# Kernel tuning notes

Hardware: AMD Instinct MI355X
Metric: run time of the kernel (lower is better)

## Reference

```python
import jax, jax.numpy as jnp
import numpy as np

B, N, D, H = 4, 2048, 256, 8
DH = D // H  # 32
EPS = 1e-5


def layernorm(x, g, b):
    mu = jnp.mean(x, axis=-1, keepdims=True)
    var = jnp.mean(jnp.square(x - mu), axis=-1, keepdims=True)
    return (x - mu) * jax.lax.rsqrt(var + EPS) * g + b


def setup_inputs() -> dict:
    key = jax.random.key(0)
    ks = jax.random.split(key, 16)
    s = 1.0 / np.sqrt(D)
    p = lambda k: jax.random.uniform(k, (D, D), jnp.float32, -s, s)
    return {
        "qdt": jax.random.normal(ks[0], (B, N, D), jnp.float32),
        "boxes": jax.random.normal(ks[1], (B, N, D), jnp.float32),
        "mask": jax.random.randint(ks[2], (N, N), 0, 2, jnp.int32),
        "Wq": p(ks[3]), "bq": jnp.zeros((D,), jnp.float32),
        "Wk": p(ks[4]), "bk": jnp.zeros((D,), jnp.float32),
        "Wv": p(ks[5]), "bv": jnp.zeros((D,), jnp.float32),
        "Wo": p(ks[6]), "bo": jnp.zeros((D,), jnp.float32),
        "W1": p(ks[7]), "b1": jnp.zeros((D,), jnp.float32),
        "W2": p(ks[8]), "b2": jnp.zeros((D,), jnp.float32),
        "g1": jnp.ones((D,), jnp.float32), "be1": jnp.zeros((D,), jnp.float32),
        "g2": jnp.ones((D,), jnp.float32), "be2": jnp.zeros((D,), jnp.float32),
    }


def reference(qdt, boxes, mask, Wq, bq, Wk, bk, Wv, bv, Wo, bo,
              W1, b1, W2, b2, g1, be1, g2, be2):
    # q = k = tgt = boxes + qdt  (dropout in eval mode -> identity)
    x = boxes + qdt  # [B,N,D]
    q = (x @ Wq + bq).reshape(B, N, H, DH)
    k = (x @ Wk + bk).reshape(B, N, H, DH)
    v = (x @ Wv + bv).reshape(B, N, H, DH)
    scores = jnp.einsum('bqhd,bkhd->bhqk', q, k) / np.sqrt(DH)
    # masked_fill(mask==0, -inf) then sigmoid  ==  sigmoid gated to 0 where masked
    attn = jnp.where(mask.astype(bool)[None, None, :, :],
                     jax.nn.sigmoid(scores), 0.0)
    o = jnp.einsum('bhqk,bkhd->bqhd', attn, v).reshape(B, N, D)
    attn_out = o @ Wo + bo
    tgt = layernorm(x + attn_out, g1, be1)
    ff = jax.nn.relu(tgt @ W1 + b1) @ W2 + b2
    tgt = layernorm(tgt + ff, g2, be2)
    return tgt
```

## Files before the change

### kernel.cpp

```cpp
#include <hip/hip_runtime.h>
#include <hip/hip_bf16.h>

typedef unsigned short u16;
typedef unsigned int u32;
typedef __attribute__((ext_vector_type(8))) short bf16x8;
typedef __attribute__((ext_vector_type(4))) float f32x4;

#define BB 4
#define NN 2048
#define DD 256
#define HH 8
#define LAMBDA 0.17677669529f

__device__ inline u16 bfu(float f) {
  __hip_bfloat16 h = __float2bfloat16(f);
  return *reinterpret_cast<u16*>(&h);
}
__device__ inline bf16x8 asfrag(uint4 v) { return __builtin_bit_cast(bf16x8, v); }

__global__ __launch_bounds__(256) void prep_kernel(
    const float* __restrict__ qdt, const float* __restrict__ boxes,
    const int* __restrict__ mask,
    const float* __restrict__ Wq, const float* __restrict__ Wk, const float* __restrict__ Wv,
    const float* __restrict__ Wo, const float* __restrict__ W1, const float* __restrict__ W2,
    const float* __restrict__ bq, const float* __restrict__ bk, const float* __restrict__ bv,
    float* __restrict__ xp, u16* __restrict__ xb, unsigned char* __restrict__ m8,
    u16* __restrict__ wqkvT, u16* __restrict__ woT, u16* __restrict__ w1T, u16* __restrict__ w2T,
    float* __restrict__ bqkv) {
  const int bid = blockIdx.x, t = threadIdx.x;
  if (bid < 2048) {
    int i = bid * 256 + t;
    int row = i >> 6, q = i & 63;
    float4 a = ((const float4*)qdt)[i];
    float4 b = ((const float4*)boxes)[i];
    float4 v = make_float4(a.x + b.x, a.y + b.y, a.z + b.z, a.w + b.w);
    ((ushort4*)xb)[i] = make_ushort4(bfu(v.x), bfu(v.y), bfu(v.z), bfu(v.w));
    float* xr = xp + (size_t)row * 256;
    xr[((4*q+0) & 15) * 16 + ((4*q+0) >> 4)] = v.x;
    xr[((4*q+1) & 15) * 16 + ((4*q+1) >> 4)] = v.y;
    xr[((4*q+2) & 15) * 16 + ((4*q+2) >> 4)] = v.z;
    xr[((4*q+3) & 15) * 16 + ((4*q+3) >> 4)] = v.w;
  } else if (bid < 6144) {
    int i = (bid - 2048) * 256 + t;
    int4 m = ((const int4*)mask)[i];
    ((uchar4*)m8)[i] = make_uchar4((unsigned char)m.x, (unsigned char)m.y,
                                   (unsigned char)m.z, (unsigned char)m.w);
  } else {
    int i = (bid - 6144) * 256 + t;
    if (i < 196608) {
      int n = i >> 8, k = i & 255;
      const float* src = (n < 256) ? Wq : (n < 512 ? Wk : Wv);
      wqkvT[i] = bfu(src[k * 256 + (n & 255)]);
    } else if (i < 262144) {
      int j = i - 196608; int n = j >> 8, k = j & 255;
      woT[j] = bfu(Wo[k * 256 + n]);
    } else if (i < 327680) {
      int j = i - 262144; int n = j >> 8, k = j & 255;
      w1T[j] = bfu(W1[k * 256 + n]);
    } else if (i < 393216) {
      int j = i - 327680; int n = j >> 8, k = j & 255;
      w2T[j] = bfu(W2[k * 256 + n]);
    } else if (i < 393984) {
      int n = i - 393216;
      bqkv[n] = (n < 256) ? bq[n] : (n < 512 ? bk[n - 256] : bv[n - 512]);
    }
  }
}

#define GEMM_BODY()                                                              \
  __shared__ u16 At[64][264];                                                    \
  __shared__ u16 Bs[64][264];                                                    \
  const int m0 = blockIdx.x * 64;                                                \
  const int n0 = blockIdx.y * 64;                                                \
  const int t = threadIdx.x;                                                     \
  {                                                                              \
    const int row = t >> 2, cb = (t & 3) * 64;                                   \
    const u16* ga = A  + (size_t)(m0 + row) * 256 + cb;                          \
    const u16* gb = Bt + (size_t)(n0 + row) * 256 + cb;                          \
    _Pragma("unroll")                                                            \
    for (int i = 0; i < 8; ++i) {                                                \
      *(int4*)&At[row][cb + i * 8] = *(const int4*)(ga + i * 8);                 \
      *(int4*)&Bs[row][cb + i * 8] = *(const int4*)(gb + i * 8);                 \
    }                                                                            \
  }                                                                              \
  __syncthreads();                                                               \
  const int w = t >> 6, l = t & 63, g = l >> 4, c = l & 15;                      \
  f32x4 acc[4] = {};                                                             \
  _Pragma("unroll")                                                              \
  for (int kk = 0; kk < 256; kk += 32) {                                         \
    bf16x8 af = *(const bf16x8*)&At[w * 16 + c][kk + g * 8];                     \
    _Pragma("unroll")                                                            \
    for (int j = 0; j < 4; ++j) {                                                \
      bf16x8 bfr = *(const bf16x8*)&Bs[j * 16 + c][kk + g * 8];                  \
      acc[j] = __builtin_amdgcn_mfma_f32_16x16x32_bf16(af, bfr, acc[j], 0, 0, 0);\
    }                                                                            \
  }

__global__ __launch_bounds__(256) void gemm_qk_kernel(
    const u16* __restrict__ A, const u16* __restrict__ Bt, const float* __restrict__ bias,
    u16* __restrict__ qout, u16* __restrict__ kout) {
  GEMM_BODY()
  if (n0 < 256) {
#pragma unroll
    for (int j = 0; j < 4; ++j)
#pragma unroll
      for (int r = 0; r < 4; ++r) {
        int m = m0 + w * 16 + g * 4 + r, n = n0 + j * 16 + c;
        qout[(size_t)m * 256 + n] = bfu((acc[j][r] + bias[n]) * LAMBDA);
      }
  } else {
#pragma unroll
    for (int j = 0; j < 4; ++j)
#pragma unroll
      for (int r = 0; r < 4; ++r) {
        int m = m0 + w * 16 + g * 4 + r, n = n0 + j * 16 + c;
        int ch = n - 256;
        kout[(size_t)((m >> 11) * 8 + (ch >> 5)) * 65536 + (size_t)(m & 2047) * 32 + (ch & 31)]
            = bfu(acc[j][r] + bias[n]);
      }
  }
}

__global__ __launch_bounds__(256) void gemm_vt_kernel(
    const u16* __restrict__ A, const u16* __restrict__ Bt, const float* __restrict__ bias,
    u16* __restrict__ vtout) {
  GEMM_BODY()
#pragma unroll
  for (int j = 0; j < 4; ++j)
#pragma unroll
    for (int r = 0; r < 4; ++r) {
      int m = m0 + w * 16 + g * 4 + r;
      int n = n0 + j * 16 + c;
      vtout[(size_t)m * 8192 + n] = bfu(acc[j][r] + bias[m]);
    }
}

__global__ __launch_bounds__(256) void attn_kernel(
    const u16* __restrict__ qb,
    const u16* __restrict__ kb,
    const u16* __restrict__ vtb,
    const unsigned char* __restrict__ m8,
    u16* __restrict__ ob) {
  __shared__ u32 Klds[2][64][20];
  __shared__ u32 Vlds[2][32][36];
  __shared__ unsigned char Mlds[2][64][64];
  __shared__ u32 Plds[4][16][36];

  const int bid = blockIdx.x;
  const int qt = bid & 31, h = (bid >> 5) & 7, b = bid >> 8;
  const int q0 = qt * 64;
  const int t = threadIdx.x, w = t >> 6, l = t & 63, g = l >> 4, c = l & 15;

  const bf16x8 qf = asfrag(*(const uint4*)(qb + (size_t)(b * NN + q0 + 16 * w + c) * 256 + h * 32 + 8 * g));
  f32x4 oacc[2] = {};

  const int srowK = t >> 2, ssegK = t & 3;
  const int srowV = t >> 3, ssegV = t & 7;
  const u16* kg = kb + (size_t)(b * 8 + h) * 65536 + srowK * 32 + ssegK * 8;
  const u16* vg = vtb + (size_t)(h * 32 + srowV) * 8192 + (size_t)b * NN + ssegV * 8;
  const unsigned char* mg = m8 + (size_t)(q0 + srowK) * NN + ssegK * 16;

  const int mb0 = (16 * ssegK + 8 * (srowK & 7)) & 63;
  const int mb1 = (mb0 + 8) & 63;

  uint4 krg = *(const uint4*)kg;
  uint4 vrg = *(const uint4*)vg;
  uint4 mrg = *(const uint4*)mg;
  *(uint4*)&Klds[0][srowK][ssegK * 4] = krg;
  *(uint4*)&Vlds[0][srowV][ssegV * 4] = vrg;
  *(uint2*)&Mlds[0][srowK][mb0] = make_uint2(mrg.x, mrg.y);
  *(uint2*)&Mlds[0][srowK][mb1] = make_uint2(mrg.z, mrg.w);
  __syncthreads();

  const f32x4 zf = {0.f, 0.f, 0.f, 0.f};
  u32* Pw = &Plds[w][0][0];

  for (int it = 0; it < 32; ++it) {
    const int cur = it & 1;
    if (it < 31) {
      const int kt = (it + 1) * 64;
      krg = *(const uint4*)(kg + (size_t)kt * 32);
      vrg = *(const uint4*)(vg + kt);
      mrg = *(const uint4*)(mg + kt);
    }
#pragma unroll
    for (int tt = 0; tt < 4; ++tt) {
      bf16x8 kf = asfrag(*(const uint4*)&Klds[cur][16 * tt + c][4 * g]);
      f32x4 s = __builtin_amdgcn_mfma_f32_16x16x32_bf16(kf, qf, zf, 0, 0, 0);
      u32 mdw = *(const u32*)&Mlds[cur][16 * w + c][(16 * tt + 4 * g + 8 * (c & 7)) & 63];
      float mf0 = (float)(mdw & 0xffu);
      float mf1 = (float)((mdw >> 8) & 0xffu);
      float mf2 = (float)((mdw >> 16) & 0xffu);
      float mf3 = (float)(mdw >> 24);
      float p0 = mf0 * __builtin_amdgcn_rcpf(1.f + __expf(-s[0]));
      float p1 = mf1 * __builtin_amdgcn_rcpf(1.f + __expf(-s[1]));
      float p2 = mf2 * __builtin_amdgcn_rcpf(1.f + __expf(-s[2]));
      float p3 = mf3 * __builtin_amdgcn_rcpf(1.f + __expf(-s[3]));
      u32 w0, w1;
      asm("v_cvt_pk_bf16_f32 %0, %1, %2" : "=v"(w0) : "v"(p0), "v"(p1));
      asm("v_cvt_pk_bf16_f32 %0, %1, %2" : "=v"(w1) : "v"(p2), "v"(p3));
      *(uint2*)&Pw[c * 36 + 8 * tt + 2 * g] = make_uint2(w0, w1);
    }
    asm volatile("s_waitcnt lgkmcnt(0)" ::: "memory");
    __builtin_amdgcn_sched_barrier(0);
#pragma unroll
    for (int kk = 0; kk < 2; ++kk) {
      bf16x8 pf = asfrag(*(const uint4*)&Pw[c * 36 + 16 * kk + 4 * g]);
#pragma unroll
      for (int d0 = 0; d0 < 2; ++d0) {
        bf16x8 vf = asfrag(*(const uint4*)&Vlds[cur][16 * d0 + c][16 * kk + 4 * g]);
        oacc[d0] = __builtin_amdgcn_mfma_f32_16x16x32_bf16(pf, vf, oacc[d0], 0, 0, 0);
      }
    }
    if (it < 31) {
      *(uint4*)&Klds[cur ^ 1][srowK][ssegK * 4] = krg;
      *(uint4*)&Vlds[cur ^ 1][srowV][ssegV * 4] = vrg;
      *(uint2*)&Mlds[cur ^ 1][srowK][mb0] = make_uint2(mrg.x, mrg.y);
      *(uint2*)&Mlds[cur ^ 1][srowK][mb1] = make_uint2(mrg.z, mrg.w);
    }
    __syncthreads();
  }

  const size_t obase = (size_t)(b * NN + q0 + 16 * w) * 256 + h * 32;
#pragma unroll
  for (int d0 = 0; d0 < 2; ++d0)
#pragma unroll
    for (int r = 0; r < 4; ++r)
      ob[obase + (size_t)(4 * g + r) * 256 + 16 * d0 + c] = bfu(oacc[d0][r]);
}

__global__ __launch_bounds__(64) void tail_kernel(
    const u16* __restrict__ obuf, const u16* __restrict__ woT,
    const u16* __restrict__ w1T, const u16* __restrict__ w2T,
    const float* __restrict__ xp,
    const float* __restrict__ bo, const float* __restrict__ b1, const float* __restrict__ b2,
    const float* __restrict__ g1, const float* __restrict__ be1,
    const float* __restrict__ g2, const float* __restrict__ be2,
    float* __restrict__ out) {
  __shared__ u16 A[16][264];
  __shared__ float T1[16][260];
  const int t = threadIdx.x, g = t >> 4, c = t & 15;
  const int m0 = blockIdx.x * 16;
  const f32x4 zf4 = {0.f, 0.f, 0.f, 0.f};

  {
    const int srow = t >> 2, sseg = t & 3;
#pragma unroll
    for (int i = 0; i < 8; ++i) {
      uint4 v = *(const uint4*)(obuf + (size_t)(m0 + srow) * 256 + (sseg + 4 * i) * 8);
      *(uint4*)&A[srow][(sseg + 4 * i) * 8] = v;
    }
  }
  asm volatile("s_waitcnt lgkmcnt(0)" ::: "memory");
  __builtin_amdgcn_sched_barrier(0);

  f32x4 acc[16];
  float s1[4], s2[4], mean[4], inv[4];

#pragma unroll
  for (int j = 0; j < 16; ++j) acc[j] = zf4;
#pragma unroll
  for (int kk = 0; kk < 256; kk += 32) {
    bf16x8 af = *(const bf16x8*)&A[c][kk + 8 * g];
#pragma unroll
    for (int j = 0; j < 16; ++j) {
      bf16x8 bfr = asfrag(*(const uint4*)(woT + (size_t)(16 * j + c) * 256 + kk + 8 * g));
      acc[j] = __builtin_amdgcn_mfma_f32_16x16x32_bf16(af, bfr, acc[j], 0, 0, 0);
    }
  }
  {
    float bov[16];
#pragma unroll
    for (int j = 0; j < 16; ++j) bov[j] = bo[16 * j + c];
#pragma unroll
    for (int r = 0; r < 4; ++r) {
      const float* xrow = xp + (size_t)(m0 + 4 * g + r) * 256 + c * 16;
      float4 xq0 = ((const float4*)xrow)[0], xq1 = ((const float4*)xrow)[1];
      float4 xq2 = ((const float4*)xrow)[2], xq3 = ((const float4*)xrow)[3];
      float xa[16] = {xq0.x, xq0.y, xq0.z, xq0.w, xq1.x, xq1.y, xq1.z, xq1.w,
                      xq2.x, xq2.y, xq2.z, xq2.w, xq3.x, xq3.y, xq3.z, xq3.w};
      float a1 = 0.f, a2 = 0.f;
#pragma unroll
      for (int j = 0; j < 16; ++j) {
        float z = acc[j][r] + bov[j] + xa[j];
        T1[4 * g + r][16 * j + c] = z;
        a1 += z; a2 += z * z;
      }
      s1[r] = a1; s2[r] = a2;
    }
  }
#pragma unroll
  for (int r = 0; r < 4; ++r) {
#pragma unroll
    for (int off = 1; off < 16; off <<= 1) {
      s1[r] += __shfl_xor(s1[r], off);
      s2[r] += __shfl_xor(s2[r], off);
    }
    mean[r] = s1[r] * (1.f / 256.f);
    inv[r] = rsqrtf(s2[r] * (1.f / 256.f) - mean[r] * mean[r] + 1e-5f);
  }
  asm volatile("s_waitcnt lgkmcnt(0)" ::: "memory");
  __builtin_amdgcn_sched_barrier(0);
#pragma unroll
  for (int j = 0; j < 16; ++j) {
    const int n = 16 * j + c;
    const float gv = g1[n], bev = be1[n];
#pragma unroll
    for (int r = 0; r < 4; ++r) {
      float v = (T1[4 * g + r][n] - mean[r]) * inv[r] * gv + bev;
      T1[4 * g + r][n] = v;
      A[4 * g + r][n] = bfu(v);
    }
  }
  asm volatile("s_waitcnt lgkmcnt(0)" ::: "memory");
  __builtin_amdgcn_sched_barrier(0);

#pragma unroll
  for (int j = 0; j < 16; ++j) acc[j] = zf4;
#pragma unroll
  for (int kk = 0; kk < 256; kk += 32) {
    bf16x8 af = *(const bf16x8*)&A[c][kk + 8 * g];
#pragma unroll
    for (int j = 0; j < 16; ++j) {
      bf16x8 bfr = asfrag(*(const uint4*)(w1T + (size_t)(16 * j + c) * 256 + kk + 8 * g));
      acc[j] = __builtin_amdgcn_mfma_f32_16x16x32_bf16(af, bfr, acc[j], 0, 0, 0);
    }
  }
  asm volatile("" ::: "memory");
  __builtin_amdgcn_sched_barrier(0);
#pragma unroll
  for (int j = 0; j < 16; ++j) {
    const int n = 16 * j + c;
    const float bv = b1[n];
#pragma unroll
    for (int r = 0; r < 4; ++r) {
      float v = acc[j][r] + bv;
      A[4 * g + r][n] = bfu(v > 0.f ? v : 0.f);
    }
  }
  asm volatile("s_waitcnt lgkmcnt(0)" ::: "memory");
  __builtin_amdgcn_sched_barrier(0);

#pragma unroll
  for (int j = 0; j < 16; ++j) acc[j] = zf4;
#pragma unroll
  for (int kk = 0; kk < 256; kk += 32) {
    bf16x8 af = *(const bf16x8*)&A[c][kk + 8 * g];
#pragma unroll
    for (int j = 0; j < 16; ++j) {
      bf16x8 bfr = asfrag(*(const uint4*)(w2T + (size_t)(16 * j + c) * 256 + kk + 8 * g));
      acc[j] = __builtin_amdgcn_mfma_f32_16x16x32_bf16(af, bfr, acc[j], 0, 0, 0);
    }
  }
  {
    float b2v[16];
#pragma unroll
    for (int j = 0; j < 16; ++j) b2v[j] = b2[16 * j + c];
#pragma unroll
    for (int r = 0; r < 4; ++r) {
      float a1 = 0.f, a2 = 0.f;
#pragma unroll
      for (int j = 0; j < 16; ++j) {
        float z = acc[j][r] + b2v[j] + T1[4 * g + r][16 * j + c];
        T1[4 * g + r][16 * j + c] = z;
        a1 += z; a2 += z * z;
      }
      s1[r] = a1; s2[r] = a2;
    }
  }
#pragma unroll
  for (int r = 0; r < 4; ++r) {
#pragma unroll
    for (int off = 1; off < 16; off <<= 1) {
      s1[r] += __shfl_xor(s1[r], off);
      s2[r] += __shfl_xor(s2[r], off);
    }
    mean[r] = s1[r] * (1.f / 256.f);
    inv[r] = rsqrtf(s2[r] * (1.f / 256.f) - mean[r] * mean[r] + 1e-5f);
  }
  asm volatile("s_waitcnt lgkmcnt(0)" ::: "memory");
  __builtin_amdgcn_sched_barrier(0);
#pragma unroll
  for (int j = 0; j < 16; ++j) {
    const int n = 16 * j + c;
    const float gv = g2[n], bev = be2[n];
#pragma unroll
    for (int r = 0; r < 4; ++r)
      out[(size_t)(m0 + 4 * g + r) * 256 + n] = (T1[4 * g + r][n] - mean[r]) * inv[r] * gv + bev;
  }
}

extern "C" void kernel_launch(void* const* d_in, const int* in_sizes, int n_in,
                              void* d_out, int out_size, void* d_ws, size_t ws_size,
                              hipStream_t stream) {
  const float* qdt   = (const float*)d_in[0];
  const float* boxes = (const float*)d_in[1];
  const int*   mask  = (const int*)d_in[2];
  const float* Wq = (const float*)d_in[3];
  const float* bq = (const float*)d_in[4];
  const float* Wk = (const float*)d_in[5];
  const float* bk = (const float*)d_in[6];
  const float* Wv = (const float*)d_in[7];
  const float* bv = (const float*)d_in[8];
  const float* Wo = (const float*)d_in[9];
  const float* bo = (const float*)d_in[10];
  const float* W1 = (const float*)d_in[11];
  const float* b1 = (const float*)d_in[12];
  const float* W2 = (const float*)d_in[13];
  const float* b2 = (const float*)d_in[14];
  const float* g1  = (const float*)d_in[15];
  const float* be1 = (const float*)d_in[16];
  const float* g2  = (const float*)d_in[17];
  const float* be2 = (const float*)d_in[18];

  char* ws = (char*)d_ws;
  float* xp    = (float*)(ws + 0);
  u16*   xb    = (u16*)  (ws + 8388608);
  u16*   qbuf  = (u16*)  (ws + 12582912);
  u16*   kbuf  = (u16*)  (ws + 16777216);
  u16*   vtbuf = (u16*)  (ws + 20971520);
  u16*   obuf  = (u16*)  (ws + 25165824);
  u16*   wqkvT = (u16*)  (ws + 46137344);
  u16*   woT   = (u16*)  (ws + 46530560);
  u16*   w1T   = (u16*)  (ws + 46661632);
  u16*   w2T   = (u16*)  (ws + 46792704);
  float* bqkv  = (float*)(ws + 46923776);
  unsigned char* m8 = (unsigned char*)(ws + 46926848);

  prep_kernel<<<7683, 256, 0, stream>>>(qdt, boxes, mask, Wq, Wk, Wv, Wo, W1, W2,
                                        bq, bk, bv, xp, xb, m8,
                                        wqkvT, woT, w1T, w2T, bqkv);
  gemm_qk_kernel<<<dim3(128, 8), 256, 0, stream>>>(xb, wqkvT, bqkv, qbuf, kbuf);
  gemm_vt_kernel<<<dim3(4, 128), 256, 0, stream>>>(wqkvT + 512 * 256, xb, bqkv + 512, vtbuf);
  attn_kernel<<<1024, 256, 0, stream>>>(qbuf, kbuf, vtbuf, m8, obuf);
  tail_kernel<<<512, 64, 0, stream>>>(obuf, woT, w1T, w2T, xp,
                                      bo, b1, b2, g1, be1, g2, be2, (float*)d_out);
}
```

Before: 128.3 us.

## Split tail kernel output columns across four waves per block

The fused tail kernel (out-proj, LayerNorm, FFN, LayerNorm) moves from one wave per 16-row block to four waves, each computing a 64-column slice of every GEMM. LayerNorm row statistics are reduced through shared-memory partial sums, and __syncthreads replaces the single-wave waitcnt fences. This cuts per-thread accumulator registers and serial MFMA chains, which should raise occupancy and latency hiding. The cost is extra block barriers and each wave reading the full A tile from LDS.

```diff
diff --git a/kernel.cpp b/kernel.cpp
--- a/kernel.cpp
+++ b/kernel.cpp
@@ -229,7 +229,7 @@
       ob[obase + (size_t)(4 * g + r) * 256 + 16 * d0 + c] = bfu(oacc[d0][r]);
 }
 
-__global__ __launch_bounds__(64) void tail_kernel(
+__global__ __launch_bounds__(256) void tail_kernel(
     const u16* __restrict__ obuf, const u16* __restrict__ woT,
     const u16* __restrict__ w1T, const u16* __restrict__ w2T,
     const float* __restrict__ xp,
@@ -239,71 +239,71 @@
     float* __restrict__ out) {
   __shared__ u16 A[16][264];
   __shared__ float T1[16][260];
-  const int t = threadIdx.x, g = t >> 4, c = t & 15;
+  __shared__ float PS1[16][4], PS2[16][4];
+  const int t = threadIdx.x, w = t >> 6, l = t & 63, g = l >> 4, c = l & 15;
   const int m0 = blockIdx.x * 16;
+  const int n0 = w * 64;
   const f32x4 zf4 = {0.f, 0.f, 0.f, 0.f};
 
   {
-    const int srow = t >> 2, sseg = t & 3;
-#pragma unroll
-    for (int i = 0; i < 8; ++i) {
-      uint4 v = *(const uint4*)(obuf + (size_t)(m0 + srow) * 256 + (sseg + 4 * i) * 8);
-      *(uint4*)&A[srow][(sseg + 4 * i) * 8] = v;
-    }
-  }
-  asm volatile("s_waitcnt lgkmcnt(0)" ::: "memory");
-  __builtin_amdgcn_sched_barrier(0);
-
-  f32x4 acc[16];
-  float s1[4], s2[4], mean[4], inv[4];
-
-#pragma unroll
-  for (int j = 0; j < 16; ++j) acc[j] = zf4;
+    const int srow = t >> 4, sseg = t & 15;
+#pragma unroll
+    for (int i = 0; i < 2; ++i) {
+      uint4 v = *(const uint4*)(obuf + (size_t)(m0 + srow) * 256 + (sseg + 16 * i) * 8);
+      *(uint4*)&A[srow][(sseg + 16 * i) * 8] = v;
+    }
+  }
+  __syncthreads();
+
+  f32x4 acc[4];
+  float mean[4], inv[4];
+
+#pragma unroll
+  for (int j = 0; j < 4; ++j) acc[j] = zf4;
 #pragma unroll
   for (int kk = 0; kk < 256; kk += 32) {
     bf16x8 af = *(const bf16x8*)&A[c][kk + 8 * g];
 #pragma unroll
-    for (int j = 0; j < 16; ++j) {
-      bf16x8 bfr = asfrag(*(const uint4*)(woT + (size_t)(16 * j + c) * 256 + kk + 8 * g));
+    for (int j = 0; j < 4; ++j) {
+      bf16x8 bfr = asfrag(*(const uint4*)(woT + (size_t)(n0 + 16 * j + c) * 256 + kk + 8 * g));
       acc[j] = __builtin_amdgcn_mfma_f32_16x16x32_bf16(af, bfr, acc[j], 0, 0, 0);
     }
   }
   {
-    float bov[16];
-#pragma unroll
-    for (int j = 0; j < 16; ++j) bov[j] = bo[16 * j + c];
+    float bov[4];
+#pragma unroll
+    for (int j = 0; j < 4; ++j) bov[j] = bo[n0 + 16 * j + c];
 #pragma unroll
     for (int r = 0; r < 4; ++r) {
-      const float* xrow = xp + (size_t)(m0 + 4 * g + r) * 256 + c * 16;
-      float4 xq0 = ((const float4*)xrow)[0], xq1 = ((const float4*)xrow)[1];
-      float4 xq2 = ((const float4*)xrow)[2], xq3 = ((const float4*)xrow)[3];
-      float xa[16] = {xq0.x, xq0.y, xq0.z, xq0.w, xq1.x, xq1.y, xq1.z, xq1.w,
-                      xq2.x, xq2.y, xq2.z, xq2.w, xq3.x, xq3.y, xq3.z, xq3.w};
+      float4 xq = ((const float4*)(xp + (size_t)(m0 + 4 * g + r) * 256 + c * 16))[w];
+      float xa[4] = {xq.x, xq.y, xq.z, xq.w};
       float a1 = 0.f, a2 = 0.f;
 #pragma unroll
-      for (int j = 0; j < 16; ++j) {
+      for (int j = 0; j < 4; ++j) {
         float z = acc[j][r] + bov[j] + xa[j];
-        T1[4 * g + r][16 * j + c] = z;
+        T1[4 * g + r][n0 + 16 * j + c] = z;
         a1 += z; a2 += z * z;
       }
-      s1[r] = a1; s2[r] = a2;
-    }
-  }
+#pragma unroll
+      for (int off = 1; off < 16; off <<= 1) {
+        a1 += __shfl_xor(a1, off);
+        a2 += __shfl_xor(a2, off);
+      }
+      if (c == 0) { PS1[4 * g + r][w] = a1; PS2[4 * g + r][w] = a2; }
+    }
+  }
+  __syncthreads();
 #pragma unroll
   for (int r = 0; r < 4; ++r) {
-#pragma unroll
-    for (int off = 1; off < 16; off <<= 1) {
-      s1[r] += __shfl_xor(s1[r], off);
-      s2[r] += __shfl_xor(s2[r], off);
-    }
-    mean[r] = s1[r] * (1.f / 256.f);
-    inv[r] = rsqrtf(s2[r] * (1.f / 256.f) - mean[r] * mean[r] + 1e-5f);
-  }
-  asm volatile("s_waitcnt lgkmcnt(0)" ::: "memory");
-  __builtin_amdgcn_sched_barrier(0);
-#pragma unroll
-  for (int j = 0; j < 16; ++j) {
-    const int n = 16 * j + c;
+    const int row = 4 * g + r;
+    float s1 = PS1[row][0] + PS1[row][1] + PS1[row][2] + PS1[row][3];
+    float s2 = PS2[row][0] + PS2[row][1] + PS2[row][2] + PS2[row][3];
+    mean[r] = s1 * (1.f / 256.f);
+    inv[r] = rsqrtf(s2 * (1.f / 256.f) - mean[r] * mean[r] + 1e-5f);
+  }
+#pragma unroll
+  for (int j = 0; j < 4; ++j) {
+    const int n = n0 + 16 * j + c;
     const float gv = g1[n], bev = be1[n];
 #pragma unroll
     for (int r = 0; r < 4; ++r) {
@@ -312,25 +312,23 @@
       A[4 * g + r][n] = bfu(v);
     }
   }
-  asm volatile("s_waitcnt lgkmcnt(0)" ::: "memory");
-  __builtin_amdgcn_sched_barrier(0);
-
-#pragma unroll
-  for (int j = 0; j < 16; ++j) acc[j] = zf4;
+  __syncthreads();
+
+#pragma unroll
+  for (int j = 0; j < 4; ++j) acc[j] = zf4;
 #pragma unroll
   for (int kk = 0; kk < 256; kk += 32) {
     bf16x8 af = *(const bf16x8*)&A[c][kk + 8 * g];
 #pragma unroll
-    for (int j = 0; j < 16; ++j) {
-      bf16x8 bfr = asfrag(*(const uint4*)(w1T + (size_t)(16 * j + c) * 256 + kk + 8 * g));
+    for (int j = 0; j < 4; ++j) {
+      bf16x8 bfr = asfrag(*(const uint4*)(w1T + (size_t)(n0 + 16 * j + c) * 256 + kk + 8 * g));
       acc[j] = __builtin_amdgcn_mfma_f32_16x16x32_bf16(af, bfr, acc[j], 0, 0, 0);
     }
   }
-  asm volatile("" ::: "memory");
-  __builtin_amdgcn_sched_barrier(0);
-#pragma unroll
-  for (int j = 0; j < 16; ++j) {
-    const int n = 16 * j + c;
+  __syncthreads();
+#pragma unroll
+  for (int j = 0; j < 4; ++j) {
+    const int n = n0 + 16 * j + c;
     const float bv = b1[n];
 #pragma unroll
     for (int r = 0; r < 4; ++r) {
@@ -338,51 +336,53 @@
       A[4 * g + r][n] = bfu(v > 0.f ? v : 0.f);
     }
   }
-  asm volatile("s_waitcnt lgkmcnt(0)" ::: "memory");
-  __builtin_amdgcn_sched_barrier(0);
-
-#pragma unroll
-  for (int j = 0; j < 16; ++j) acc[j] = zf4;
+  __syncthreads();
+
+#pragma unroll
+  for (int j = 0; j < 4; ++j) acc[j] = zf4;
 #pragma unroll
   for (int kk = 0; kk < 256; kk += 32) {
     bf16x8 af = *(const bf16x8*)&A[c][kk + 8 * g];
 #pragma unroll
-    for (int j = 0; j < 16; ++j) {
-      bf16x8 bfr = asfrag(*(const uint4*)(w2T + (size_t)(16 * j + c) * 256 + kk + 8 * g));
+    for (int j = 0; j < 4; ++j) {
+      bf16x8 bfr = asfrag(*(const uint4*)(w2T + (size_t)(n0 + 16 * j + c) * 256 + kk + 8 * g));
       acc[j] = __builtin_amdgcn_mfma_f32_16x16x32_bf16(af, bfr, acc[j], 0, 0, 0);
     }
   }
   {
-    float b2v[16];
-#pragma unroll
-    for (int j = 0; j < 16; ++j) b2v[j] = b2[16 * j + c];
+    float b2v[4];
+#pragma unroll
+    for (int j = 0; j < 4; ++j) b2v[j] = b2[n0 + 16 * j + c];
 #pragma unroll
     for (int r = 0; r < 4; ++r) {
       float a1 = 0.f, a2 = 0.f;
 #pragma unroll
-      for (int j = 0; j < 16; ++j) {
-        float z = acc[j][r] + b2v[j] + T1[4 * g + r][16 * j + c];
-        T1[4 * g + r][16 * j + c] = z;
+      for (int j = 0; j < 4; ++j) {
+        const int n = n0 + 16 * j + c;
+        float z = acc[j][r] + b2v[j] + T1[4 * g + r][n];
+        T1[4 * g + r][n] = z;
         a1 += z; a2 += z * z;
       }
-      s1[r] = a1; s2[r] = a2;
-    }
-  }
+#pragma unroll
+      for (int off = 1; off < 16; off <<= 1) {
+        a1 += __shfl_xor(a1, off);
+        a2 += __shfl_xor(a2, off);
+      }
+      if (c == 0) { PS1[4 * g + r][w] = a1; PS2[4 * g + r][w] = a2; }
+    }
+  }
+  __syncthreads();
 #pragma unroll
   for (int r = 0; r < 4; ++r) {
-#pragma unroll
-    for (int off = 1; off < 16; off <<= 1) {
-      s1[r] += __shfl_xor(s1[r], off);
-      s2[r] += __shfl_xor(s2[r], off);
-    }
-    mean[r] = s1[r] * (1.f / 256.f);
-    inv[r] = rsqrtf(s2[r] * (1.f / 256.f) - mean[r] * mean[r] + 1e-5f);
-  }
-  asm volatile("s_waitcnt lgkmcnt(0)" ::: "memory");
-  __builtin_amdgcn_sched_barrier(0);
-#pragma unroll
-  for (int j = 0; j < 16; ++j) {
-    const int n = 16 * j + c;
+    const int row = 4 * g + r;
+    float s1 = PS1[row][0] + PS1[row][1] + PS1[row][2] + PS1[row][3];
+    float s2 = PS2[row][0] + PS2[row][1] + PS2[row][2] + PS2[row][3];
+    mean[r] = s1 * (1.f / 256.f);
+    inv[r] = rsqrtf(s2 * (1.f / 256.f) - mean[r] * mean[r] + 1e-5f);
+  }
+#pragma unroll
+  for (int j = 0; j < 4; ++j) {
+    const int n = n0 + 16 * j + c;
     const float gv = g2[n], bev = be2[n];
 #pragma unroll
     for (int r = 0; r < 4; ++r)
@@ -433,6 +433,6 @@
   gemm_qk_kernel<<<dim3(128, 8), 256, 0, stream>>>(xb, wqkvT, bqkv, qbuf, kbuf);
   gemm_vt_kernel<<<dim3(4, 128), 256, 0, stream>>>(wqkvT + 512 * 256, xb, bqkv + 512, vtbuf);
   attn_kernel<<<1024, 256, 0, stream>>>(qbuf, kbuf, vtbuf, m8, obuf);
-  tail_kernel<<<512, 64, 0, stream>>>(obuf, woT, w1T, w2T, xp,
-                                      bo, b1, b2, g1, be1, g2, be2, (float*)d_out);
-}
+  tail_kernel<<<512, 256, 0, stream>>>(obuf, woT, w1T, w2T, xp,
+                                       bo, b1, b2, g1, be1, g2, be2, (float*)d_out);
+}
```

Result: faster. 117.6 us (-8.4%).
